# Optimization experiments

Hardware: AMD Instinct MI355X
Metric: run time of the kernel (lower is better)

Reference implementation:

```python
import jax, jax.numpy as jnp
import numpy as np

GRID_SIZE = 4
SPLINE_ORDER = 3
EDGE_DIM = 384


def make_grid():
    # efficient-KAN default grid_range [-1, 1]
    h = 2.0 / GRID_SIZE
    return (jnp.arange(-SPLINE_ORDER, GRID_SIZE + SPLINE_ORDER + 1, dtype=jnp.float32) * h - 1.0)


def b_splines(x, grid, k):
    # x: (N, d); grid: (G+2k+1,) shared across features -> (N, d, G+k)
    xe = x[..., None]
    bases = ((xe >= grid[:-1]) & (xe < grid[1:])).astype(x.dtype)
    for j in range(1, k + 1):
        bases = ((xe - grid[: -(j + 1)]) / (grid[j:-1] - grid[: -(j + 1)]) * bases[..., :-1]
                 + (grid[j + 1:] - xe) / (grid[j + 1:] - grid[1:-j]) * bases[..., 1:])
    return bases


def kan_linear(x, base_W, spline_W, grid):
    # efficient-KAN KANLinear: silu base path + spline path
    base = jax.nn.silu(x) @ base_W.T
    B = b_splines(x, grid, SPLINE_ORDER)          # (N, in, G+k)
    spline = jnp.einsum('nic,oic->no', B, spline_W)
    return base + spline


def gckan_layer(x, edge_index, edge_attr, p, grid):
    ea = edge_attr @ p['edge_W'].T + p['edge_b']          # (E, out)
    xt = x @ p['node_W'].T + p['node_b']                  # (N, out)
    row, col = edge_index[0], edge_index[1]
    msg = ea * xt[row]                                    # gather + multiply
    agg = jnp.zeros_like(xt).at[col].add(msg)             # scatter-add
    return kan_linear(agg, p['base_W'], p['spline_W'], grid)


def _layer_params(key, in_feat, out_feat):
    k1, k2, k3, k4 = jax.random.split(key, 4)
    coef = GRID_SIZE + SPLINE_ORDER
    return {
        'node_W': jax.random.normal(k1, (out_feat, in_feat), jnp.float32) / np.sqrt(in_feat),
        'node_b': jnp.zeros((out_feat,), jnp.float32),
        'edge_W': jax.random.normal(k2, (out_feat, EDGE_DIM), jnp.float32) / np.sqrt(EDGE_DIM),
        'edge_b': jnp.zeros((out_feat,), jnp.float32),
        'base_W': jax.random.normal(k3, (out_feat, out_feat), jnp.float32) / np.sqrt(out_feat),
        'spline_W': jax.random.normal(k4, (out_feat, out_feat, coef), jnp.float32) * (0.1 / np.sqrt(out_feat)),
    }


def setup_inputs() -> dict:
    N, E, F, H, C = 50000, 500000, 256, 256, 32
    key = jax.random.key(0)
    ks = jax.random.split(key, 6)
    inp = {
        'x': jax.random.normal(ks[0], (N, F), jnp.float32),
        'edge_index': jax.random.randint(ks[1], (2, E), 0, N, jnp.int32),
        'edge_attr': jax.random.normal(ks[2], (E, EDGE_DIM), jnp.float32),
    }
    p0 = _layer_params(ks[3], F, H)
    p1 = _layer_params(ks[4], H, H)
    po = _layer_params(ks[5], F + 2 * H, C)
    for tag, p in (('0', p0), ('1', p1), ('o', po)):
        for n, v in p.items():
            inp[n + tag] = v
    return inp


def reference(x, edge_index, edge_attr,
              node_W0, node_b0, edge_W0, edge_b0, base_W0, spline_W0,
              node_W1, node_b1, edge_W1, edge_b1, base_W1, spline_W1,
              node_Wo, node_bo, edge_Wo, edge_bo, base_Wo, spline_Wo):
    grid = make_grid()
    p0 = dict(node_W=node_W0, node_b=node_b0, edge_W=edge_W0, edge_b=edge_b0, base_W=base_W0, spline_W=spline_W0)
    p1 = dict(node_W=node_W1, node_b=node_b1, edge_W=edge_W1, edge_b=edge_b1, base_W=base_W1, spline_W=spline_W1)
    po = dict(node_W=node_Wo, node_b=node_bo, edge_W=edge_Wo, edge_b=edge_bo, base_W=base_Wo, spline_W=spline_Wo)
    skips = [x]
    h = gckan_layer(x, edge_index, edge_attr, p0, grid)
    skips.append(h)
    h = gckan_layer(h, edge_index, edge_attr, p1, grid)
    skips.append(h)
    h = jnp.concatenate(skips, axis=1)  # skip=True concat -> (N, F+2H)
    return gckan_layer(h, edge_index, edge_attr, po, grid)
```

## Files before the change

### kernel.cpp

```cpp
#include <hip/hip_runtime.h>


typedef __attribute__((ext_vector_type(4))) float f32x4;
typedef __attribute__((ext_vector_type(8))) short bf16x8;
typedef __attribute__((ext_vector_type(8))) unsigned short u16x8;
typedef __attribute__((ext_vector_type(4))) unsigned short u16x4;

__device__ __forceinline__ unsigned short f2bf(float f) {
    union { float f; unsigned u; } v; v.f = f;
    unsigned r = v.u + 0x7FFFu + ((v.u >> 16) & 1u);
    return (unsigned short)(r >> 16);
}

__device__ __forceinline__ float bf2f(unsigned short u) {
    union { unsigned u; float f; } v; v.u = ((unsigned)u) << 16;
    return v.f;
}

__device__ __forceinline__ float siluf(float x) {
    return x / (1.0f + __expf(-x));
}

__device__ __forceinline__ void gl16(const void* g, void* l) {
    __builtin_amdgcn_global_load_lds(
        (const __attribute__((address_space(1))) unsigned*)g,
        (__attribute__((address_space(3))) unsigned*)l, 16, 0, 0);
}

__device__ __forceinline__ void expand8(float x, float* o8) {
    float b[10];
#pragma unroll
    for (int i = 0; i < 10; ++i) {
        float ti = 0.5f * i - 2.5f;
        b[i] = (x >= ti && x < ti + 0.5f) ? 1.0f : 0.0f;
    }
#pragma unroll
    for (int j = 1; j <= 3; ++j) {
        float inv = 2.0f / (float)j;
#pragma unroll
        for (int i = 0; i < 10 - j; ++i) {
            float ti = 0.5f * i - 2.5f;
            float tj = 0.5f * (i + j + 1) - 2.5f;
            b[i] = (x - ti) * inv * b[i] + (tj - x) * inv * b[i + 1];
        }
    }
    o8[0] = siluf(x);
#pragma unroll
    for (int c = 0; c < 7; ++c) o8[c + 1] = b[c];
}

__global__ __launch_bounds__(256) void k_hist(
    const int* __restrict__ col, int* __restrict__ cnt, int E) {
    int i = blockIdx.x * 256 + threadIdx.x;
    if (i < E) atomicAdd(&cnt[col[i]], 1);
}

__global__ __launch_bounds__(1024) void k_scan(int* __restrict__ c, int N) {
    __shared__ int wsum[16];
    __shared__ int ctot;
    const int t = threadIdx.x;
    const int lane = t & 63, wid = t >> 6;
    int carry = 0;
    for (int base = 0; base < N; base += 1024) {
        int i = base + t;
        int v0 = (i < N) ? c[i] : 0;
        int v = v0;
#pragma unroll
        for (int off = 1; off < 64; off <<= 1) {
            int n = __shfl_up(v, (unsigned)off, 64);
            if (lane >= off) v += n;
        }
        if (lane == 63) wsum[wid] = v;
        __syncthreads();
        if (t < 16) {
            int s = wsum[t], sv = s;
#pragma unroll
            for (int off = 1; off < 16; off <<= 1) {
                int n = __shfl_up(sv, (unsigned)off, 16);
                if (t >= off) sv += n;
            }
            wsum[t] = sv - s;
            if (t == 15) ctot = sv;
        }
        __syncthreads();
        if (i < N) c[i] = carry + wsum[wid] + v - v0;
        carry += ctot;
        __syncthreads();
    }
}

__global__ __launch_bounds__(256) void k_scatter(
    const int* __restrict__ row, const int* __restrict__ col,
    int* __restrict__ cursor, int* __restrict__ rowS,
    int* __restrict__ colS, int* __restrict__ posS, int E) {
    int i = blockIdx.x * 256 + threadIdx.x;
    if (i < E) {
        int c = col[i];
        int p = atomicAdd(&cursor[c], 1);
        rowS[p] = row[i];
        colS[p] = c;
        posS[i] = p;
    }
}

template <bool TWO, bool WITH_O>
__global__ __launch_bounds__(256, 2) void ea_gemm2(
    const float* __restrict__ EA,
    const unsigned short* __restrict__ W0, const float* __restrict__ b0,
    const unsigned short* __restrict__ W1, const float* __restrict__ b1,
    const unsigned short* __restrict__ Wo, const float* __restrict__ bo,
    const int* __restrict__ posS,
    unsigned short* __restrict__ O0, unsigned short* __restrict__ O1,
    unsigned short* __restrict__ Oo, int E) {
    constexpr int BOOFF = TWO ? 73728 : 40960;
    constexpr int SMEMSZ = BOOFF + (WITH_O ? 4096 : 0);
    __shared__ __align__(16) char smem[SMEMSZ];
    __shared__ int pos_s[64];

    const int tid = threadIdx.x;
    const int wv = tid >> 6, lane = tid & 63;
    const int l15 = lane & 15, l4 = lane >> 4;
    const long m0 = (long)blockIdx.x * 64;

    f32x4 acc0[4][4] = {};
    f32x4 acc1[4][4] = {};
    f32x4 acco[4] = {};

    const int sr = tid >> 2, sg = tid & 3;
    const long arow = m0 + sr;
    const bool aok = arow < E;
    const float* aptr = EA + arow * 384 + sg * 8;
    const int awoff = sg * 1024 + ((sr ^ (sg << 2))) * 16;

    const unsigned short* w0p = W0 + (long)tid * 384;
    const unsigned short* w1p = TWO ? (W1 + (long)tid * 384) : W0;
    const unsigned short* wop = Wo;
    if (WITH_O) {
        int o = wv * 1024 + lane * 16;
        int g = o >> 9, brow = (o >> 4) & 31;
        wop = Wo + (long)brow * 384 + g * 8;
    }

    if (tid < 64) { long p = m0 + tid; pos_s[tid] = (p < E) ? posS[p] : -1; }

#define ISSUE_B(IT, BUF)                                                       \
    {                                                                          \
        _Pragma("unroll")                                                      \
        for (int g = 0; g < 4; ++g)                                            \
            gl16(w0p + (IT) * 32 + g * 8,                                      \
                 smem + 8192 + (BUF) * 16384 + g * 4096 + wv * 1024);          \
        if (TWO) {                                                             \
            _Pragma("unroll")                                                  \
            for (int g = 0; g < 4; ++g)                                        \
                gl16(w1p + (IT) * 32 + g * 8,                                  \
                     smem + 40960 + (BUF) * 16384 + g * 4096 + wv * 1024);     \
        }                                                                      \
        if (WITH_O && wv < 2)                                                  \
            gl16(wop + (IT) * 32, smem + BOOFF + (BUF) * 2048 + wv * 1024);    \
        __builtin_amdgcn_sched_barrier(0);                                     \
    }

#define WRITE_A(BUF)                                                           \
    {                                                                          \
        u16x8 rr = {};                                                         \
        if (aok) {                                                             \
            rr[0] = f2bf(a0v.x); rr[1] = f2bf(a0v.y);                          \
            rr[2] = f2bf(a0v.z); rr[3] = f2bf(a0v.w);                          \
            rr[4] = f2bf(a1v.x); rr[5] = f2bf(a1v.y);                          \
            rr[6] = f2bf(a1v.z); rr[7] = f2bf(a1v.w);                          \
        }                                                                      \
        *(u16x8*)(smem + (BUF) * 4096 + awoff) = rr;                           \
        __builtin_amdgcn_sched_barrier(0);                                     \
    }

    ISSUE_B(0, 0);
    float4 a0v = make_float4(0.f, 0.f, 0.f, 0.f);
    float4 a1v = make_float4(0.f, 0.f, 0.f, 0.f);
    if (aok) { a0v = *(const float4*)(aptr); a1v = *(const float4*)(aptr + 4); }
    WRITE_A(0);
    if (aok) { a0v = *(const float4*)(aptr + 32); a1v = *(const float4*)(aptr + 36); }
    __builtin_amdgcn_sched_barrier(0);

#pragma unroll
    for (int it = 0; it < 12; ++it) {
        if (it == 11) asm volatile("s_waitcnt vmcnt(0)" ::: "memory");
        else          asm volatile("s_waitcnt vmcnt(2)" ::: "memory");
        asm volatile("s_waitcnt lgkmcnt(0)" ::: "memory");
        __builtin_amdgcn_s_barrier();
        __builtin_amdgcn_sched_barrier(0);
        const int buf = it & 1, nbf = buf ^ 1;
        if (it < 11) {
            ISSUE_B(it + 1, nbf);
            WRITE_A(nbf);
            if (it < 10) {
                if (aok) {
                    a0v = *(const float4*)(aptr + (it + 2) * 32);
                    a1v = *(const float4*)(aptr + (it + 2) * 32 + 4);
                }
                __builtin_amdgcn_sched_barrier(0);
            }
        }
        bf16x8 af[4];
#pragma unroll
        for (int mi = 0; mi < 4; ++mi)
            af[mi] = *(const bf16x8*)(smem + buf * 4096 + l4 * 1024 +
                                      (((mi * 16 + l15) ^ (l4 << 2))) * 16);
        {
            bf16x8 bf0[4];
#pragma unroll
            for (int nj = 0; nj < 4; ++nj)
                bf0[nj] = *(const bf16x8*)(smem + 8192 + buf * 16384 + l4 * 4096 +
                                           (wv * 64 + nj * 16 + l15) * 16);
#pragma unroll
            for (int mi = 0; mi < 4; ++mi)
#pragma unroll
                for (int nj = 0; nj < 4; ++nj)
                    acc0[mi][nj] = __builtin_amdgcn_mfma_f32_16x16x32_bf16(
                        af[mi], bf0[nj], acc0[mi][nj], 0, 0, 0);
        }
        if (TWO) {
            bf16x8 bf1[4];
#pragma unroll
            for (int nj = 0; nj < 4; ++nj)
                bf1[nj] = *(const bf16x8*)(smem + 40960 + buf * 16384 + l4 * 4096 +
                                           (wv * 64 + nj * 16 + l15) * 16);
#pragma unroll
            for (int mi = 0; mi < 4; ++mi)
#pragma unroll
                for (int nj = 0; nj < 4; ++nj)
                    acc1[mi][nj] = __builtin_amdgcn_mfma_f32_16x16x32_bf16(
                        af[mi], bf1[nj], acc1[mi][nj], 0, 0, 0);
        }
        if (WITH_O && wv < 2) {
            bf16x8 bov = *(const bf16x8*)(smem + BOOFF + buf * 2048 + l4 * 512 +
                                          (wv * 16 + l15) * 16);
#pragma unroll
            for (int mi = 0; mi < 4; ++mi)
                acco[mi] = __builtin_amdgcn_mfma_f32_16x16x32_bf16(
                    af[mi], bov, acco[mi], 0, 0, 0);
        }
    }
#undef ISSUE_B
#undef WRITE_A

    const int nb2 = wv * 64;
    float bs0[4];
#pragma unroll
    for (int nj = 0; nj < 4; ++nj) bs0[nj] = b0[nb2 + nj * 16 + l15];
#pragma unroll
    for (int mi = 0; mi < 4; ++mi) {
#pragma unroll
        for (int r = 0; r < 4; ++r) {
            int edge = mi * 16 + l4 * 4 + r;
            int pos = pos_s[edge];
            if (pos >= 0) {
                unsigned short* dst = O0 + (long)pos * 256 + nb2 + l15;
#pragma unroll
                for (int nj = 0; nj < 4; ++nj)
                    dst[nj * 16] = f2bf(acc0[mi][nj][r] + bs0[nj]);
            }
        }
    }
    if (TWO) {
        float bs1[4];
#pragma unroll
        for (int nj = 0; nj < 4; ++nj) bs1[nj] = b1[nb2 + nj * 16 + l15];
#pragma unroll
        for (int mi = 0; mi < 4; ++mi) {
#pragma unroll
            for (int r = 0; r < 4; ++r) {
                int edge = mi * 16 + l4 * 4 + r;
                int pos = pos_s[edge];
                if (pos >= 0) {
                    unsigned short* dst = O1 + (long)pos * 256 + nb2 + l15;
#pragma unroll
                    for (int nj = 0; nj < 4; ++nj)
                        dst[nj * 16] = f2bf(acc1[mi][nj][r] + bs1[nj]);
                }
            }
        }
    }
    if (WITH_O && wv < 2) {
        float bso = bo[wv * 16 + l15];
#pragma unroll
        for (int mi = 0; mi < 4; ++mi) {
#pragma unroll
            for (int r = 0; r < 4; ++r) {
                int edge = mi * 16 + l4 * 4 + r;
                int pos = pos_s[edge];
                if (pos >= 0)
                    Oo[(long)pos * 32 + wv * 16 + l15] = f2bf(acco[mi][r] + bso);
            }
        }
    }
}

__global__ __launch_bounds__(256) void msg256(
    const unsigned short* __restrict__ EAr, const unsigned short* __restrict__ XT,
    const int* __restrict__ rowS, const int* __restrict__ colS,
    float* __restrict__ AGG, int E) {
    __shared__ __align__(16) unsigned short eas[64][256];
    __shared__ int rows_s[64];
    __shared__ int cols_s[64];
    const int tid = threadIdx.x;
    const int wv = tid >> 6, lane = tid & 63;
    const long m0 = (long)blockIdx.x * 64;

    const char* src = (const char*)(EAr + m0 * 256);
#pragma unroll
    for (int j = 0; j < 8; ++j)
        gl16(src + (j * 4 + wv) * 1024 + lane * 16,
             ((char*)&eas[0][0]) + (j * 4 + wv) * 1024);
    if (tid < 64) {
        long p = m0 + tid;
        cols_s[tid] = (p < E) ? colS[p] : -1;
        rows_s[tid] = (p < E) ? rowS[p] : 0;
    }
    __syncthreads();

    const int c = tid;
    float sum = 0.f;
    int cur = cols_s[0];
    int runstart = 0;
#pragma unroll 1
    for (int g = 0; g < 8; ++g) {
        float xv[8];
#pragma unroll
        for (int j = 0; j < 8; ++j)
            xv[j] = bf2f(XT[(long)rows_s[g * 8 + j] * 256 + c]);
#pragma unroll
        for (int j = 0; j < 8; ++j) {
            int e = g * 8 + j;
            int cc = cols_s[e];
            if (cc != cur) {
                if (cur >= 0) {
                    float* dst = AGG + (long)cur * 256 + c;
                    if (runstart > 0) *dst = sum;
                    else atomicAdd(dst, sum);
                }
                cur = cc; runstart = e; sum = 0.f;
            }
            sum += bf2f(eas[e][c]) * xv[j];
        }
    }
    if (cur >= 0) {
        atomicAdd(AGG + (long)cur * 256 + c, sum);
    }
}

__global__ __launch_bounds__(256) void msg32(
    const unsigned short* __restrict__ EAro, const unsigned short* __restrict__ XT,
    const int* __restrict__ rowS, const int* __restrict__ colS,
    float* __restrict__ AGG, int E) {
    __shared__ __align__(16) unsigned short eas[256][32];
    __shared__ int rows_s[256];
    __shared__ int cols_s[256];
    const int tid = threadIdx.x;
    const int wv = tid >> 6, lane = tid & 63;
    const long m0 = (long)blockIdx.x * 256;

    const char* src = (const char*)(EAro + m0 * 32);
#pragma unroll
    for (int j = 0; j < 4; ++j)
        gl16(src + (j * 4 + wv) * 1024 + lane * 16,
             ((char*)&eas[0][0]) + (j * 4 + wv) * 1024);
    {
        long p = m0 + tid;
        cols_s[tid] = (p < E) ? colS[p] : -1;
        rows_s[tid] = (p < E) ? rowS[p] : 0;
    }
    __syncthreads();

    const int c = tid & 31, s = tid >> 5;
    const int e0 = s * 32;
    float sum = 0.f;
    int cur = cols_s[e0];
    int runstart = e0;
#pragma unroll 1
    for (int g = 0; g < 4; ++g) {
        float xv[8];
#pragma unroll
        for (int j = 0; j < 8; ++j)
            xv[j] = bf2f(XT[(long)rows_s[e0 + g * 8 + j] * 32 + c]);
#pragma unroll
        for (int j = 0; j < 8; ++j) {
            int e = e0 + g * 8 + j;
            int cc = cols_s[e];
            if (cc != cur) {
                if (cur >= 0) {
                    float* dst = AGG + (long)cur * 32 + c;
                    if (runstart > 0 && cols_s[runstart - 1] != cur) *dst = sum;
                    else atomicAdd(dst, sum);
                }
                cur = cc; runstart = e; sum = 0.f;
            }
            sum += bf2f(eas[e][c]) * xv[j];
        }
    }
    if (cur >= 0) {
        int eend = e0 + 32;
        float* dst = AGG + (long)cur * 32 + c;
        bool oks = (runstart > 0 && cols_s[runstart - 1] != cur);
        bool oke = (eend < 256 && cols_s[eend] != cur);
        if (oks && oke) *dst = sum;
        else atomicAdd(dst, sum);
    }
}

template <int K>
__global__ __launch_bounds__(256) void node_mfma(
    const float* __restrict__ X, const unsigned short* __restrict__ Wh,
    const float* __restrict__ bias, unsigned short* __restrict__ Y, int M) {
    __shared__ __align__(16) unsigned short As[4][64][8];
    __shared__ __align__(16) unsigned short Bs[4][256][8];
    const int tid = threadIdx.x;
    const int wv = tid >> 6, lane = tid & 63;
    const int l15 = lane & 15, l4 = lane >> 4;
    const long m0 = (long)blockIdx.x * 64;
    f32x4 acc[4][4] = {};

    const int sr = tid >> 2, sg = tid & 3;
    const long arow = m0 + sr;
    const float* aptr = X + arow * K + sg * 8;
    const bool aok = arow < M;
    const unsigned short* bptr = Wh + (long)tid * K;

    for (int it = 0; it < K / 32; ++it) {
        const int k0 = it * 32;
        u16x8 ap = {};
        if (aok) {
            float4 v0 = *(const float4*)(aptr + k0);
            float4 v1 = *(const float4*)(aptr + k0 + 4);
            ap[0] = f2bf(v0.x); ap[1] = f2bf(v0.y); ap[2] = f2bf(v0.z); ap[3] = f2bf(v0.w);
            ap[4] = f2bf(v1.x); ap[5] = f2bf(v1.y); ap[6] = f2bf(v1.z); ap[7] = f2bf(v1.w);
        }
        u16x8 b0 = *(const u16x8*)(bptr + k0);
        u16x8 b1 = *(const u16x8*)(bptr + k0 + 8);
        u16x8 b2 = *(const u16x8*)(bptr + k0 + 16);
        u16x8 b3 = *(const u16x8*)(bptr + k0 + 24);
        __syncthreads();
        *(u16x8*)&As[sg][sr][0] = ap;
        *(u16x8*)&Bs[0][tid][0] = b0;
        *(u16x8*)&Bs[1][tid][0] = b1;
        *(u16x8*)&Bs[2][tid][0] = b2;
        *(u16x8*)&Bs[3][tid][0] = b3;
        __syncthreads();
        bf16x8 af[4], bfv[4];
#pragma unroll
        for (int mi = 0; mi < 4; ++mi)
            af[mi] = *(const bf16x8*)&As[l4][mi * 16 + l15][0];
#pragma unroll
        for (int nj = 0; nj < 4; ++nj)
            bfv[nj] = *(const bf16x8*)&Bs[l4][wv * 64 + nj * 16 + l15][0];
#pragma unroll
        for (int mi = 0; mi < 4; ++mi)
#pragma unroll
            for (int nj = 0; nj < 4; ++nj)
                acc[mi][nj] = __builtin_amdgcn_mfma_f32_16x16x32_bf16(
                    af[mi], bfv[nj], acc[mi][nj], 0, 0, 0);
    }

    const int nb = wv * 64;
    float bs[4];
#pragma unroll
    for (int nj = 0; nj < 4; ++nj) bs[nj] = bias[nb + nj * 16 + l15];
#pragma unroll
    for (int mi = 0; mi < 4; ++mi) {
#pragma unroll
        for (int r = 0; r < 4; ++r) {
            long gm = m0 + mi * 16 + l4 * 4 + r;
            if (gm < M) {
#pragma unroll
                for (int nj = 0; nj < 4; ++nj)
                    Y[gm * 256 + nb + nj * 16 + l15] = f2bf(acc[mi][nj][r] + bs[nj]);
            }
        }
    }
}

__global__ __launch_bounds__(256) void kan_mfma256(
    const float* __restrict__ AGG, const unsigned short* __restrict__ Wch,
    float* __restrict__ Y, int M) {
    __shared__ __align__(16) unsigned short As[4][64][8];
    __shared__ __align__(16) unsigned short Bs[4][256][8];
    const int tid = threadIdx.x;
    const int wv = tid >> 6, lane = tid & 63;
    const int l15 = lane & 15, l4 = lane >> 4;
    const long m0 = (long)blockIdx.x * 64;
    f32x4 acc[4][4] = {};

    const int srow = tid & 63, sg = tid >> 6;
    const long arow = m0 + srow;
    const bool aok = arow < M;
    const float* aptr = AGG + arow * 256 + sg;
    const unsigned short* bptr = Wch + (long)tid * 2048;

    float xv = aok ? aptr[0] : 0.f;
    u16x8 pb0 = *(const u16x8*)(bptr);
    u16x8 pb1 = *(const u16x8*)(bptr + 8);
    u16x8 pb2 = *(const u16x8*)(bptr + 16);
    u16x8 pb3 = *(const u16x8*)(bptr + 24);

    for (int it = 0; it < 64; ++it) {
        float e8[8];
        expand8(xv, e8);
        u16x8 ap;
#pragma unroll
        for (int c = 0; c < 8; ++c) ap[c] = f2bf(e8[c]);
        __syncthreads();
        *(u16x8*)&As[sg][srow][0] = ap;
        *(u16x8*)&Bs[0][tid][0] = pb0;
        *(u16x8*)&Bs[1][tid][0] = pb1;
        *(u16x8*)&Bs[2][tid][0] = pb2;
        *(u16x8*)&Bs[3][tid][0] = pb3;
        __syncthreads();
        if (it < 63) {
            xv = aok ? aptr[(it + 1) * 4] : 0.f;
            const int k0 = (it + 1) * 32;
            pb0 = *(const u16x8*)(bptr + k0);
            pb1 = *(const u16x8*)(bptr + k0 + 8);
            pb2 = *(const u16x8*)(bptr + k0 + 16);
            pb3 = *(const u16x8*)(bptr + k0 + 24);
        }
        bf16x8 af[4], bfv[4];
#pragma unroll
        for (int mi = 0; mi < 4; ++mi)
            af[mi] = *(const bf16x8*)&As[l4][mi * 16 + l15][0];
#pragma unroll
        for (int nj = 0; nj < 4; ++nj)
            bfv[nj] = *(const bf16x8*)&Bs[l4][wv * 64 + nj * 16 + l15][0];
#pragma unroll
        for (int mi = 0; mi < 4; ++mi)
#pragma unroll
            for (int nj = 0; nj < 4; ++nj)
                acc[mi][nj] = __builtin_amdgcn_mfma_f32_16x16x32_bf16(
                    af[mi], bfv[nj], acc[mi][nj], 0, 0, 0);
    }

    const int nb = wv * 64;
#pragma unroll
    for (int mi = 0; mi < 4; ++mi) {
#pragma unroll
        for (int r = 0; r < 4; ++r) {
            long gm = m0 + mi * 16 + l4 * 4 + r;
            if (gm < M) {
#pragma unroll
                for (int nj = 0; nj < 4; ++nj)
                    Y[gm * 256 + nb + nj * 16 + l15] = acc[mi][nj][r];
            }
        }
    }
}

__global__ __launch_bounds__(256) void node_cat_mfma(
    const float* __restrict__ X, const float* __restrict__ H0,
    const float* __restrict__ H1, const unsigned short* __restrict__ Wh,
    const float* __restrict__ bias, unsigned short* __restrict__ Y, int M) {
    __shared__ __align__(16) unsigned short As[4][256][8];
    __shared__ __align__(16) unsigned short Bs[4][32][8];
    const int tid = threadIdx.x;
    const int wv = tid >> 6, lane = tid & 63;
    const int l15 = lane & 15, l4 = lane >> 4;
    const long m0 = (long)blockIdx.x * 256;
    f32x4 acc[4][2] = {};

    const int sr = tid >> 3;
    const int sq = (tid & 7) * 4;
    const int sg2 = sq >> 3, so2 = sq & 7;

    for (int it = 0; it < 24; ++it) {
        const int k0 = it * 32;
        const float* src = (it < 8) ? X : (it < 16) ? H0 : H1;
        const int kk = k0 & 255;
        float4 va[8];
#pragma unroll
        for (int j = 0; j < 8; ++j) {
            long r_ = m0 + j * 32 + sr;
            va[j] = (r_ < M) ? *(const float4*)(src + r_ * 256 + kk + sq)
                             : make_float4(0.f, 0.f, 0.f, 0.f);
        }
        u16x8 bv = {};
        if (tid < 128)
            bv = *(const u16x8*)(Wh + (long)(tid >> 2) * 768 + k0 + (tid & 3) * 8);
        __syncthreads();
#pragma unroll
        for (int j = 0; j < 8; ++j) {
            u16x4 ap;
            ap[0] = f2bf(va[j].x); ap[1] = f2bf(va[j].y);
            ap[2] = f2bf(va[j].z); ap[3] = f2bf(va[j].w);
            *(u16x4*)&As[sg2][j * 32 + sr][so2] = ap;
        }
        if (tid < 128) *(u16x8*)&Bs[tid & 3][tid >> 2][0] = bv;
        __syncthreads();
        bf16x8 af[4], bfv[2];
#pragma unroll
        for (int mi = 0; mi < 4; ++mi)
            af[mi] = *(const bf16x8*)&As[l4][wv * 64 + mi * 16 + l15][0];
#pragma unroll
        for (int nj = 0; nj < 2; ++nj)
            bfv[nj] = *(const bf16x8*)&Bs[l4][nj * 16 + l15][0];
#pragma unroll
        for (int mi = 0; mi < 4; ++mi)
#pragma unroll
            for (int nj = 0; nj < 2; ++nj)
                acc[mi][nj] = __builtin_amdgcn_mfma_f32_16x16x32_bf16(
                    af[mi], bfv[nj], acc[mi][nj], 0, 0, 0);
    }

#pragma unroll
    for (int mi = 0; mi < 4; ++mi) {
#pragma unroll
        for (int r = 0; r < 4; ++r) {
            long gm = m0 + wv * 64 + mi * 16 + l4 * 4 + r;
            if (gm < M) {
#pragma unroll
                for (int nj = 0; nj < 2; ++nj) {
                    int o = nj * 16 + l15;
                    Y[gm * 32 + o] = f2bf(acc[mi][nj][r] + bias[o]);
                }
            }
        }
    }
}

__global__ __launch_bounds__(256) void kan_gemm32(
    const float* __restrict__ AGG, const float* __restrict__ Wc,
    float* __restrict__ Y, int M) {
    __shared__ float As[64][36];
    __shared__ float Bs[32][36];
    const int tid = threadIdx.x;
    const int tx = tid & 15, ty = tid >> 4;
    const int m0 = blockIdx.x * 64;
    float acc[4][2] = {{0.f, 0.f}, {0.f, 0.f}, {0.f, 0.f}, {0.f, 0.f}};
    const int er = tid >> 2, ef = tid & 3;
    const int em = m0 + er;
    for (int ic = 0; ic < 32; ic += 4) {
        float xv = (em < M) ? AGG[(long)em * 32 + ic + ef] : 0.f;
        float e8[8];
        expand8(xv, e8);
        *(float4*)&As[er][ef * 8] = make_float4(e8[0], e8[1], e8[2], e8[3]);
        *(float4*)&As[er][ef * 8 + 4] = make_float4(e8[4], e8[5], e8[6], e8[7]);
        {
            int o = tid >> 3, k4 = (tid & 7) * 4;
            *(float4*)&Bs[o][k4] = *(const float4*)&Wc[(long)o * 256 + ic * 8 + k4];
        }
        __syncthreads();
#pragma unroll
        for (int kk = 0; kk < 32; ++kk) {
            float a_[4], b_[2];
#pragma unroll
            for (int i = 0; i < 4; ++i) a_[i] = As[ty * 4 + i][kk];
#pragma unroll
            for (int j = 0; j < 2; ++j) b_[j] = Bs[tx * 2 + j][kk];
#pragma unroll
            for (int i = 0; i < 4; ++i)
#pragma unroll
                for (int j = 0; j < 2; ++j) acc[i][j] = fmaf(a_[i], b_[j], acc[i][j]);
        }
        __syncthreads();
    }
#pragma unroll
    for (int i = 0; i < 4; ++i) {
        int gm = m0 + ty * 4 + i;
        if (gm >= M) continue;
#pragma unroll
        for (int j = 0; j < 2; ++j) Y[(long)gm * 32 + tx * 2 + j] = acc[i][j];
    }
}

__global__ __launch_bounds__(256) void cvt_bf16(
    const float* __restrict__ s, unsigned short* __restrict__ d, int n) {
    int i = blockIdx.x * 256 + threadIdx.x;
    if (i < n) d[i] = f2bf(s[i]);
}

__global__ __launch_bounds__(256) void pack_kan_bf16(
    const float* __restrict__ baseW, const float* __restrict__ splineW,
    unsigned short* __restrict__ Wc, int n) {
    int idx = blockIdx.x * 256 + threadIdx.x;
    if (idx >= n) return;
    unsigned short* dst = Wc + (long)idx * 8;
    dst[0] = f2bf(baseW[idx]);
    const float* sw = splineW + (long)idx * 7;
#pragma unroll
    for (int c = 0; c < 7; ++c) dst[1 + c] = f2bf(sw[c]);
}

__global__ __launch_bounds__(256) void pack_kan_f32(
    const float* __restrict__ baseW, const float* __restrict__ splineW,
    float* __restrict__ Wc, int n) {
    int idx = blockIdx.x * 256 + threadIdx.x;
    if (idx >= n) return;
    float* dst = Wc + (long)idx * 8;
    dst[0] = baseW[idx];
    const float* sw = splineW + (long)idx * 7;
#pragma unroll
    for (int c = 0; c < 7; ++c) dst[1 + c] = sw[c];
}

extern "C" void kernel_launch(void* const* d_in, const int* in_sizes, int n_in,
                              void* d_out, int out_size, void* d_ws, size_t ws_size,
                              hipStream_t stream) {
    const float* x          = (const float*)d_in[0];
    const int*   edge_index = (const int*)d_in[1];
    const float* edge_attr  = (const float*)d_in[2];
    const float* node_W0 = (const float*)d_in[3];
    const float* node_b0 = (const float*)d_in[4];
    const float* edge_W0 = (const float*)d_in[5];
    const float* edge_b0 = (const float*)d_in[6];
    const float* base_W0 = (const float*)d_in[7];
    const float* spline_W0 = (const float*)d_in[8];
    const float* node_W1 = (const float*)d_in[9];
    const float* node_b1 = (const float*)d_in[10];
    const float* edge_W1 = (const float*)d_in[11];
    const float* edge_b1 = (const float*)d_in[12];
    const float* base_W1 = (const float*)d_in[13];
    const float* spline_W1 = (const float*)d_in[14];
    const float* node_Wo = (const float*)d_in[15];
    const float* node_bo = (const float*)d_in[16];
    const float* edge_Wo = (const float*)d_in[17];
    const float* edge_bo = (const float*)d_in[18];
    const float* base_Wo = (const float*)d_in[19];
    const float* spline_Wo = (const float*)d_in[20];
    float* out = (float*)d_out;

    const int N = in_sizes[0] / 256;
    const int E = in_sizes[1] / 2;

    float* ws  = (float*)d_ws;
    unsigned short* xt = (unsigned short*)ws;
    float* agg = ws + (long)N * 256;
    float* h0  = agg + (long)N * 256;
    float* h1  = h0 + (long)N * 256;
    float* Wco = h1 + (long)N * 256;
    unsigned short* Wc0h = (unsigned short*)(Wco + 32 * 256);
    unsigned short* Wc1h = Wc0h + 256 * 2048;
    unsigned short* eW0h = Wc1h + 256 * 2048;
    unsigned short* eW1h = eW0h + 256 * 384;
    unsigned short* eWoh = eW1h + 256 * 384;
    unsigned short* nW0h = eWoh + 32 * 384;
    unsigned short* nW1h = nW0h + 256 * 256;
    unsigned short* nWoh = nW1h + 256 * 256;
    int* cursor = (int*)(nWoh + 32 * 768);
    int* rowS   = cursor + (N + 1);
    int* colS   = rowS + E;
    int* posS   = colS + E;
    unsigned short* EAr0 = (unsigned short*)(((uintptr_t)(posS + E) + 255) & ~(uintptr_t)255);
    const int nt256 = (E + 255) / 256;
    const long Epad = (long)nt256 * 256;
    unsigned short* EAr1 = EAr0 + Epad * 256;

    const size_t need2 = (size_t)((char*)(EAr1 + Epad * 256 + Epad * 32) - (char*)d_ws);
    const bool two = ws_size >= need2;
    unsigned short* EAro = two ? (EAr1 + Epad * 256) : (EAr0 + Epad * 256);

    const int* row = edge_index;
    const int* col = edge_index + E;

    const int nb64 = (N + 63) / 64;
    const int eb64 = (E + 63) / 64;
    const int eb256 = (E + 255) / 256;
    const int nb256 = (N + 255) / 256;

    hipMemsetAsync(cursor, 0, (size_t)(N + 1) * sizeof(int), stream);
    k_hist<<<eb256, 256, 0, stream>>>(col, cursor, E);
    k_scan<<<1, 1024, 0, stream>>>(cursor, N);
    k_scatter<<<eb256, 256, 0, stream>>>(row, col, cursor, rowS, colS, posS, E);

    cvt_bf16<<<(256 * 384 + 255) / 256, 256, 0, stream>>>(edge_W0, eW0h, 256 * 384);
    cvt_bf16<<<(256 * 384 + 255) / 256, 256, 0, stream>>>(edge_W1, eW1h, 256 * 384);
    cvt_bf16<<<(32 * 384 + 255) / 256, 256, 0, stream>>>(edge_Wo, eWoh, 32 * 384);
    cvt_bf16<<<(256 * 256 + 255) / 256, 256, 0, stream>>>(node_W0, nW0h, 256 * 256);
    cvt_bf16<<<(256 * 256 + 255) / 256, 256, 0, stream>>>(node_W1, nW1h, 256 * 256);
    cvt_bf16<<<(32 * 768 + 255) / 256, 256, 0, stream>>>(node_Wo, nWoh, 32 * 768);
    pack_kan_bf16<<<(256 * 256 + 255) / 256, 256, 0, stream>>>(base_W0, spline_W0, Wc0h, 256 * 256);
    pack_kan_bf16<<<(256 * 256 + 255) / 256, 256, 0, stream>>>(base_W1, spline_W1, Wc1h, 256 * 256);
    pack_kan_f32<<<(32 * 32 + 255) / 256, 256, 0, stream>>>(base_Wo, spline_Wo, Wco, 32 * 32);

    if (two) {
        ea_gemm2<true, true><<<eb64, 256, 0, stream>>>(
            edge_attr, eW0h, edge_b0, eW1h, edge_b1, eWoh, edge_bo,
            posS, EAr0, EAr1, EAro, E);
    } else {
        ea_gemm2<false, true><<<eb64, 256, 0, stream>>>(
            edge_attr, eW0h, edge_b0, eW0h, edge_b0, eWoh, edge_bo,
            posS, EAr0, EAr0, EAro, E);
    }

    hipMemsetAsync(agg, 0, (size_t)N * 256 * sizeof(float), stream);
    node_mfma<256><<<nb64, 256, 0, stream>>>(x, nW0h, node_b0, xt, N);
    msg256<<<eb64, 256, 0, stream>>>(EAr0, xt, rowS, colS, agg, E);
    kan_mfma256<<<nb64, 256, 0, stream>>>(agg, Wc0h, h0, N);

    if (!two) {
        ea_gemm2<false, false><<<eb64, 256, 0, stream>>>(
            edge_attr, eW1h, edge_b1, eW1h, edge_b1, eWoh, edge_bo,
            posS, EAr0, EAr0, EAro, E);
    }
    hipMemsetAsync(agg, 0, (size_t)N * 256 * sizeof(float), stream);
    node_mfma<256><<<nb64, 256, 0, stream>>>(h0, nW1h, node_b1, xt, N);
    msg256<<<eb64, 256, 0, stream>>>(two ? EAr1 : EAr0, xt, rowS, colS, agg, E);
    kan_mfma256<<<nb64, 256, 0, stream>>>(agg, Wc1h, h1, N);

    hipMemsetAsync(agg, 0, (size_t)N * 32 * sizeof(float), stream);
    node_cat_mfma<<<nb256, 256, 0, stream>>>(x, h0, h1, nWoh, node_bo, xt, N);
    msg32<<<eb256, 256, 0, stream>>>(EAro, xt, rowS, colS, agg, E);
    kan_gemm32<<<nb64, 256, 0, stream>>>(agg, Wco, out, N);
}
```

Baseline: 1.643 ms.

## Write edge projections in original order and gather by sorted edge id

The edge-attribute GEMM now stores its outputs in original edge order, so each row is written contiguously instead of scattered to the CSR-sorted position. The message kernels receive a sorted-to-original edge-id array and gather each edge row with vector loads, replacing the contiguous async LDS copy. Padded LDS rows are added to reduce bank conflicts. This swaps scattered writes in the GEMM for random reads in the message kernels, which run twice for the 256-wide layers and once for the 32-wide layer.

```diff
diff --git a/kernel.cpp b/kernel.cpp
--- a/kernel.cpp
+++ b/kernel.cpp
@@ -92,30 +92,28 @@
 __global__ __launch_bounds__(256) void k_scatter(
     const int* __restrict__ row, const int* __restrict__ col,
     int* __restrict__ cursor, int* __restrict__ rowS,
-    int* __restrict__ colS, int* __restrict__ posS, int E) {
+    int* __restrict__ colS, int* __restrict__ eidS, int E) {
     int i = blockIdx.x * 256 + threadIdx.x;
     if (i < E) {
         int c = col[i];
         int p = atomicAdd(&cursor[c], 1);
         rowS[p] = row[i];
         colS[p] = c;
-        posS[i] = p;
+        eidS[p] = i;
     }
 }
 
 template <bool TWO, bool WITH_O>
-__global__ __launch_bounds__(256, 2) void ea_gemm2(
+__global__ __launch_bounds__(256, 2) void ea_gemm3(
     const float* __restrict__ EA,
     const unsigned short* __restrict__ W0, const float* __restrict__ b0,
     const unsigned short* __restrict__ W1, const float* __restrict__ b1,
     const unsigned short* __restrict__ Wo, const float* __restrict__ bo,
-    const int* __restrict__ posS,
     unsigned short* __restrict__ O0, unsigned short* __restrict__ O1,
     unsigned short* __restrict__ Oo, int E) {
     constexpr int BOOFF = TWO ? 73728 : 40960;
     constexpr int SMEMSZ = BOOFF + (WITH_O ? 4096 : 0);
     __shared__ __align__(16) char smem[SMEMSZ];
-    __shared__ int pos_s[64];
 
     const int tid = threadIdx.x;
     const int wv = tid >> 6, lane = tid & 63;
@@ -140,8 +138,6 @@
         int g = o >> 9, brow = (o >> 4) & 31;
         wop = Wo + (long)brow * 384 + g * 8;
     }
-
-    if (tid < 64) { long p = m0 + tid; pos_s[tid] = (p < E) ? posS[p] : -1; }
 
 #define ISSUE_B(IT, BUF)                                                       \
     {                                                                          \
@@ -251,10 +247,9 @@
     for (int mi = 0; mi < 4; ++mi) {
 #pragma unroll
         for (int r = 0; r < 4; ++r) {
-            int edge = mi * 16 + l4 * 4 + r;
-            int pos = pos_s[edge];
-            if (pos >= 0) {
-                unsigned short* dst = O0 + (long)pos * 256 + nb2 + l15;
+            long e = m0 + mi * 16 + l4 * 4 + r;
+            if (e < E) {
+                unsigned short* dst = O0 + e * 256 + nb2 + l15;
 #pragma unroll
                 for (int nj = 0; nj < 4; ++nj)
                     dst[nj * 16] = f2bf(acc0[mi][nj][r] + bs0[nj]);
@@ -269,10 +264,9 @@
         for (int mi = 0; mi < 4; ++mi) {
 #pragma unroll
             for (int r = 0; r < 4; ++r) {
-                int edge = mi * 16 + l4 * 4 + r;
-                int pos = pos_s[edge];
-                if (pos >= 0) {
-                    unsigned short* dst = O1 + (long)pos * 256 + nb2 + l15;
+                long e = m0 + mi * 16 + l4 * 4 + r;
+                if (e < E) {
+                    unsigned short* dst = O1 + e * 256 + nb2 + l15;
 #pragma unroll
                     for (int nj = 0; nj < 4; ++nj)
                         dst[nj * 16] = f2bf(acc1[mi][nj][r] + bs1[nj]);
@@ -286,10 +280,9 @@
         for (int mi = 0; mi < 4; ++mi) {
 #pragma unroll
             for (int r = 0; r < 4; ++r) {
-                int edge = mi * 16 + l4 * 4 + r;
-                int pos = pos_s[edge];
-                if (pos >= 0)
-                    Oo[(long)pos * 32 + wv * 16 + l15] = f2bf(acco[mi][r] + bso);
+                long e = m0 + mi * 16 + l4 * 4 + r;
+                if (e < E)
+                    Oo[e * 32 + wv * 16 + l15] = f2bf(acco[mi][r] + bso);
             }
         }
     }
@@ -298,19 +291,27 @@
 __global__ __launch_bounds__(256) void msg256(
     const unsigned short* __restrict__ EAr, const unsigned short* __restrict__ XT,
     const int* __restrict__ rowS, const int* __restrict__ colS,
-    float* __restrict__ AGG, int E) {
-    __shared__ __align__(16) unsigned short eas[64][256];
+    const int* __restrict__ eidS, float* __restrict__ AGG, int E) {
+    __shared__ __align__(16) unsigned short eas[64][264];
     __shared__ int rows_s[64];
     __shared__ int cols_s[64];
     const int tid = threadIdx.x;
-    const int wv = tid >> 6, lane = tid & 63;
     const long m0 = (long)blockIdx.x * 64;
 
-    const char* src = (const char*)(EAr + m0 * 256);
-#pragma unroll
-    for (int j = 0; j < 8; ++j)
-        gl16(src + (j * 4 + wv) * 1024 + lane * 16,
-             ((char*)&eas[0][0]) + (j * 4 + wv) * 1024);
+    const int r = tid >> 2, s = tid & 3;
+    {
+        long p = m0 + r;
+        if (p < E) {
+            const unsigned short* src = EAr + (long)eidS[p] * 256 + s * 8;
+#pragma unroll
+            for (int k = 0; k < 8; ++k)
+                *(u16x8*)&eas[r][s * 8 + k * 32] = *(const u16x8*)(src + k * 32);
+        } else {
+            u16x8 z = {};
+#pragma unroll
+            for (int k = 0; k < 8; ++k) *(u16x8*)&eas[r][s * 8 + k * 32] = z;
+        }
+    }
     if (tid < 64) {
         long p = m0 + tid;
         cols_s[tid] = (p < E) ? colS[p] : -1;
@@ -351,28 +352,34 @@
 __global__ __launch_bounds__(256) void msg32(
     const unsigned short* __restrict__ EAro, const unsigned short* __restrict__ XT,
     const int* __restrict__ rowS, const int* __restrict__ colS,
-    float* __restrict__ AGG, int E) {
-    __shared__ __align__(16) unsigned short eas[256][32];
+    const int* __restrict__ eidS, float* __restrict__ AGG, int E) {
+    __shared__ __align__(16) unsigned short eas[256][36];
     __shared__ int rows_s[256];
     __shared__ int cols_s[256];
+    __shared__ int eid_s[256];
     const int tid = threadIdx.x;
-    const int wv = tid >> 6, lane = tid & 63;
     const long m0 = (long)blockIdx.x * 256;
 
-    const char* src = (const char*)(EAro + m0 * 32);
-#pragma unroll
-    for (int j = 0; j < 4; ++j)
-        gl16(src + (j * 4 + wv) * 1024 + lane * 16,
-             ((char*)&eas[0][0]) + (j * 4 + wv) * 1024);
     {
         long p = m0 + tid;
         cols_s[tid] = (p < E) ? colS[p] : -1;
         rows_s[tid] = (p < E) ? rowS[p] : 0;
+        eid_s[tid]  = (p < E) ? eidS[p] : -1;
     }
     __syncthreads();
-
-    const int c = tid & 31, s = tid >> 5;
-    const int e0 = s * 32;
+    const int rr0 = tid >> 2, s = tid & 3;
+#pragma unroll
+    for (int ps = 0; ps < 4; ++ps) {
+        int rr = ps * 64 + rr0;
+        int eid = eid_s[rr];
+        u16x8 v = {};
+        if (eid >= 0) v = *(const u16x8*)(EAro + (long)eid * 32 + s * 8);
+        *(u16x8*)&eas[rr][s * 8] = v;
+    }
+    __syncthreads();
+
+    const int c = tid & 31, sb = tid >> 5;
+    const int e0 = sb * 32;
     float sum = 0.f;
     int cur = cols_s[e0];
     int runstart = e0;
@@ -744,8 +751,8 @@
     int* cursor = (int*)(nWoh + 32 * 768);
     int* rowS   = cursor + (N + 1);
     int* colS   = rowS + E;
-    int* posS   = colS + E;
-    unsigned short* EAr0 = (unsigned short*)(((uintptr_t)(posS + E) + 255) & ~(uintptr_t)255);
+    int* eidS   = colS + E;
+    unsigned short* EAr0 = (unsigned short*)(((uintptr_t)(eidS + E) + 255) & ~(uintptr_t)255);
     const int nt256 = (E + 255) / 256;
     const long Epad = (long)nt256 * 256;
     unsigned short* EAr1 = EAr0 + Epad * 256;
@@ -765,7 +772,7 @@
     hipMemsetAsync(cursor, 0, (size_t)(N + 1) * sizeof(int), stream);
     k_hist<<<eb256, 256, 0, stream>>>(col, cursor, E);
     k_scan<<<1, 1024, 0, stream>>>(cursor, N);
-    k_scatter<<<eb256, 256, 0, stream>>>(row, col, cursor, rowS, colS, posS, E);
+    k_scatter<<<eb256, 256, 0, stream>>>(row, col, cursor, rowS, colS, eidS, E);
 
     cvt_bf16<<<(256 * 384 + 255) / 256, 256, 0, stream>>>(edge_W0, eW0h, 256 * 384);
     cvt_bf16<<<(256 * 384 + 255) / 256, 256, 0, stream>>>(edge_W1, eW1h, 256 * 384);
@@ -778,32 +785,32 @@
     pack_kan_f32<<<(32 * 32 + 255) / 256, 256, 0, stream>>>(base_Wo, spline_Wo, Wco, 32 * 32);
 
     if (two) {
-        ea_gemm2<true, true><<<eb64, 256, 0, stream>>>(
+        ea_gemm3<true, true><<<eb64, 256, 0, stream>>>(
             edge_attr, eW0h, edge_b0, eW1h, edge_b1, eWoh, edge_bo,
-            posS, EAr0, EAr1, EAro, E);
+            EAr0, EAr1, EAro, E);
     } else {
-        ea_gemm2<false, true><<<eb64, 256, 0, stream>>>(
+        ea_gemm3<false, true><<<eb64, 256, 0, stream>>>(
             edge_attr, eW0h, edge_b0, eW0h, edge_b0, eWoh, edge_bo,
-            posS, EAr0, EAr0, EAro, E);
+            EAr0, EAr0, EAro, E);
     }
 
     hipMemsetAsync(agg, 0, (size_t)N * 256 * sizeof(float), stream);
     node_mfma<256><<<nb64, 256, 0, stream>>>(x, nW0h, node_b0, xt, N);
-    msg256<<<eb64, 256, 0, stream>>>(EAr0, xt, rowS, colS, agg, E);
+    msg256<<<eb64, 256, 0, stream>>>(EAr0, xt, rowS, colS, eidS, agg, E);
     kan_mfma256<<<nb64, 256, 0, stream>>>(agg, Wc0h, h0, N);
 
     if (!two) {
-        ea_gemm2<false, false><<<eb64, 256, 0, stream>>>(
+        ea_gemm3<false, false><<<eb64, 256, 0, stream>>>(
             edge_attr, eW1h, edge_b1, eW1h, edge_b1, eWoh, edge_bo,
-            posS, EAr0, EAr0, EAro, E);
+            EAr0, EAr0, EAro, E);
     }
     hipMemsetAsync(agg, 0, (size_t)N * 256 * sizeof(float), stream);
     node_mfma<256><<<nb64, 256, 0, stream>>>(h0, nW1h, node_b1, xt, N);
-    msg256<<<eb64, 256, 0, stream>>>(two ? EAr1 : EAr0, xt, rowS, colS, agg, E);
+    msg256<<<eb64, 256, 0, stream>>>(two ? EAr1 : EAr0, xt, rowS, colS, eidS, agg, E);
     kan_mfma256<<<nb64, 256, 0, stream>>>(agg, Wc1h, h1, N);
 
     hipMemsetAsync(agg, 0, (size_t)N * 32 * sizeof(float), stream);
     node_cat_mfma<<<nb256, 256, 0, stream>>>(x, h0, h1, nWoh, node_bo, xt, N);
-    msg32<<<eb256, 256, 0, stream>>>(EAro, xt, rowS, colS, agg, E);
+    msg32<<<eb256, 256, 0, stream>>>(EAro, xt, rowS, colS, eidS, agg, E);
     kan_gemm32<<<nb64, 256, 0, stream>>>(agg, Wco, out, N);
 }
```

Result: no change. 1.674 ms (+1.8%).
